# Optimization experiments

Hardware: AMD Instinct MI355X
Metric: run time of the kernel (lower is better)

Reference implementation:

```python
import jax, jax.numpy as jnp
import numpy as np

EPS_CR = 0.5      # eps in coding rate
ETA = 0.5
LAMBDA_LAP = 0.3
LN_EPS = 1e-5


def setup_inputs() -> dict:
    key = jax.random.key(0)
    ks = jax.random.split(key, 8)
    n, in_dim, out_dim, d_sub, K1 = 8192, 256, 128, 64, 3
    H = jax.random.normal(ks[0], (n, in_dim), jnp.float32)
    hop_feats = jax.random.normal(ks[1], (K1, n, in_dim), jnp.float32)
    L = jax.random.normal(ks[2], (n, n), jnp.float32) * 0.01
    W_stack = jax.random.normal(ks[3], (K1, d_sub, in_dim), jnp.float32) * 0.05
    W_out = jax.random.normal(ks[4], (out_dim, in_dim), jnp.float32) * 0.05
    threshold = jnp.full((out_dim,), 0.05, jnp.float32)
    ln_gamma = jnp.ones((out_dim,), jnp.float32)
    ln_beta = jnp.zeros((out_dim,), jnp.float32)
    tau = jnp.asarray(1.0, jnp.float32)
    return {"H": H, "hop_feats": hop_feats, "L": L, "W_stack": W_stack,
            "W_out": W_out, "threshold": threshold, "ln_gamma": ln_gamma,
            "ln_beta": ln_beta, "tau": tau}


def reference(H, hop_feats, L, W_stack, W_out, threshold, ln_gamma, ln_beta, tau):
    n = H.shape[0]
    d = W_stack.shape[1]
    coeff = d / (n * EPS_CR * EPS_CR)
    # per-hop subspace projections: Z [K+1, n, d]
    Z = jnp.einsum('knf,kdf->knd', hop_feats, W_stack)
    # shared Gram M = I + coeff * Z^T Z  [K+1, d, d]
    G = jnp.einsum('knd,kne->kde', Z, Z)
    M = jnp.eye(d, dtype=Z.dtype)[None] + coeff * G
    # coding rates via batched slogdet
    _, logdet = jnp.linalg.slogdet(M)
    R = 0.5 * logdet                                    # [K+1]
    # delta_R: first entry is R[0], rest are successive diffs
    delta_R = R - jnp.concatenate([jnp.zeros((1,), R.dtype), R[:-1]])
    dR_norm = (delta_R - delta_R.mean()) / (jnp.std(delta_R, ddof=1) + 1e-6)
    w = jax.nn.softmax(dR_norm / tau)                   # [K+1]
    # coding-rate gradients: g_Z = coeff * Z @ M^{-1} via batched solve
    g_Z = coeff * jnp.linalg.solve(M, jnp.swapaxes(Z, 1, 2))  # [K+1, d, n]
    # g_H[k] = g_Z[k]^T @ W[k]; weighted sum over hops -> [n, in_dim]
    grad_contrib = jnp.einsum('k,kdn,kdf->nf', w, g_Z, W_stack)
    H_half = H + ETA * grad_contrib - ETA * LAMBDA_LAP * (L @ H)
    # in_dim != out_dim -> project
    H_pre = H_half @ W_out.T                            # [n, out_dim]
    thr = jnp.abs(threshold)[None, :]
    H_soft = jnp.sign(H_pre) * jnp.maximum(jnp.abs(H_pre) - thr, 0.0)
    # LayerNorm over last dim
    mu = H_soft.mean(-1, keepdims=True)
    var = jnp.mean((H_soft - mu) ** 2, -1, keepdims=True)
    H_out = (H_soft - mu) * jax.lax.rsqrt(var + LN_EPS) * ln_gamma + ln_beta
    return (H_out, w, jax.lax.stop_gradient(dR_norm), jax.lax.stop_gradient(delta_R))
```

## Files before the change

kernel.cpp:

```cpp
#include <hip/hip_runtime.h>
#include <hip/hip_bf16.h>
#include <math.h>


#define COEFF 0.03125f
#define SCL_LAP (-0.15f)

typedef __attribute__((ext_vector_type(8))) short short8;
typedef __attribute__((ext_vector_type(4))) float f32x4;

__device__ __forceinline__ unsigned short f2bf_bits(float f) {
  unsigned int u = __float_as_uint(f);
  unsigned int r = (u + 0x7fffu + ((u >> 16) & 1u)) >> 16;
  return (unsigned short)r;
}

__global__ __launch_bounds__(256) void front_kernel(
    const float* __restrict__ H, const float* __restrict__ hop,
    const float* __restrict__ Wst, const float* __restrict__ Wout,
    float* __restrict__ Hp, unsigned short* __restrict__ HpT,
    float* __restrict__ Zbuf, float* __restrict__ Gpart,
    float* __restrict__ Pb) {
  __shared__ __align__(16) float smem[8704];
  float* As = smem;
  float* Bs = smem + 2112;
  const int tid = threadIdx.x;
  const int tx = tid & 15, ty = tid >> 4;
  const int b = blockIdx.x;

  const float* A;
  const float* B;
  int m0 = 0, k_id = 0, n_off = 0, mode;
  if (b < 192) {
    mode = 0; k_id = b >> 6; m0 = (b & 63) * 128;
    A = hop + (size_t)k_id * 2097152;
    B = Wst + (size_t)k_id * 16384;
  } else if (b < 320) {
    mode = 1; int i2 = b - 192;
    m0 = (i2 >> 1) * 128; n_off = (i2 & 1) * 64;
    A = H; B = Wout + (size_t)n_off * 256;
  } else {
    mode = 2; k_id = b - 320; m0 = 0;
    A = Wout; B = Wst + (size_t)k_id * 16384;
  }

  float acc[8][4];
#pragma unroll
  for (int i = 0; i < 8; ++i)
#pragma unroll
    for (int j = 0; j < 4; ++j) acc[i][j] = 0.f;

  const int arow = tid >> 1, ak = (tid & 1) * 8;
  const int brow = tid >> 2, bk = (tid & 3) * 4;
  for (int k0 = 0; k0 < 256; k0 += 16) {
    float4 a0 = *(const float4*)(A + (size_t)(m0 + arow) * 256 + k0 + ak);
    float4 a1 = *(const float4*)(A + (size_t)(m0 + arow) * 256 + k0 + ak + 4);
    float4 bv = *(const float4*)(B + (size_t)brow * 256 + k0 + bk);
    __syncthreads();
    As[(ak + 0) * 132 + arow] = a0.x; As[(ak + 1) * 132 + arow] = a0.y;
    As[(ak + 2) * 132 + arow] = a0.z; As[(ak + 3) * 132 + arow] = a0.w;
    As[(ak + 4) * 132 + arow] = a1.x; As[(ak + 5) * 132 + arow] = a1.y;
    As[(ak + 6) * 132 + arow] = a1.z; As[(ak + 7) * 132 + arow] = a1.w;
    Bs[(bk + 0) * 68 + brow] = bv.x; Bs[(bk + 1) * 68 + brow] = bv.y;
    Bs[(bk + 2) * 68 + brow] = bv.z; Bs[(bk + 3) * 68 + brow] = bv.w;
    __syncthreads();
#pragma unroll
    for (int kk = 0; kk < 16; ++kk) {
      float4 x0 = *(const float4*)&As[kk * 132 + ty * 8];
      float4 x1 = *(const float4*)&As[kk * 132 + ty * 8 + 4];
      float4 y4 = *(const float4*)&Bs[kk * 68 + tx * 4];
      float a8[8] = {x0.x, x0.y, x0.z, x0.w, x1.x, x1.y, x1.z, x1.w};
      float b4[4] = {y4.x, y4.y, y4.z, y4.w};
#pragma unroll
      for (int i = 0; i < 8; ++i)
#pragma unroll
        for (int j = 0; j < 4; ++j) acc[i][j] = fmaf(a8[i], b4[j], acc[i][j]);
    }
  }
  __syncthreads();

  if (mode == 0) {
#pragma unroll
    for (int i = 0; i < 8; ++i) {
      float4 v = {acc[i][0], acc[i][1], acc[i][2], acc[i][3]};
      *(float4*)(Zbuf + (size_t)(m0 + ty * 8 + i) * 192 + k_id * 64 + tx * 4) = v;
      *(float4*)&smem[(ty * 8 + i) * 68 + tx * 4] = v;
    }
    __syncthreads();
    float g[4][4];
#pragma unroll
    for (int i = 0; i < 4; ++i)
#pragma unroll
      for (int j = 0; j < 4; ++j) g[i][j] = 0.f;
    for (int r = 0; r < 128; ++r) {
      float4 zd4 = *(const float4*)&smem[r * 68 + ty * 4];
      float4 ze4 = *(const float4*)&smem[r * 68 + tx * 4];
      float zd[4] = {zd4.x, zd4.y, zd4.z, zd4.w};
      float ze[4] = {ze4.x, ze4.y, ze4.z, ze4.w};
#pragma unroll
      for (int i = 0; i < 4; ++i)
#pragma unroll
        for (int j = 0; j < 4; ++j) g[i][j] = fmaf(zd[i], ze[j], g[i][j]);
    }
    float* gp = Gpart + (size_t)(k_id * 64 + (b & 63)) * 4096;
#pragma unroll
    for (int i = 0; i < 4; ++i) {
      float4 v = {g[i][0], g[i][1], g[i][2], g[i][3]};
      *(float4*)(gp + (ty * 4 + i) * 64 + tx * 4) = v;
    }
  } else if (mode == 1) {
#pragma unroll
    for (int i = 0; i < 8; ++i) {
      float4 v = {acc[i][0], acc[i][1], acc[i][2], acc[i][3]};
      *(float4*)(Hp + (size_t)(m0 + ty * 8 + i) * 128 + n_off + tx * 4) = v;
      *(float4*)&smem[(ty * 8 + i) * 68 + tx * 4] = v;
    }
    __syncthreads();
    const int nn = tid >> 2, mc = (tid & 3) * 32;
    __attribute__((aligned(16))) unsigned short tmp[32];
#pragma unroll
    for (int mm = 0; mm < 32; ++mm) tmp[mm] = f2bf_bits(smem[(mc + mm) * 68 + nn]);
    unsigned short* dst = HpT + (size_t)(n_off + nn) * 8192 + m0 + mc;
    *(uint4*)(dst) = *(const uint4*)&tmp[0];
    *(uint4*)(dst + 8) = *(const uint4*)&tmp[8];
    *(uint4*)(dst + 16) = *(const uint4*)&tmp[16];
    *(uint4*)(dst + 24) = *(const uint4*)&tmp[24];
  } else {
    float* P = Pb + (size_t)k_id * 8192;
#pragma unroll
    for (int i = 0; i < 8; ++i) {
      float4 v = {acc[i][0], acc[i][1], acc[i][2], acc[i][3]};
      *(float4*)(P + (size_t)(ty * 8 + i) * 64 + tx * 4) = v;
    }
  }
}

__device__ __forceinline__ float blocksum256(float v, volatile float* scr) {
#pragma unroll
  for (int o = 32; o; o >>= 1) v += __shfl_xor(v, o);
  __syncthreads();
  if ((threadIdx.x & 63) == 0) scr[threadIdx.x >> 6] = v;
  __syncthreads();
  return scr[0] + scr[1] + scr[2] + scr[3];
}

__device__ __forceinline__ void gemm64s(const float* X, const float* Y,
                                        float acc[4][4]) {
  const int tx = threadIdx.x & 15, ty = threadIdx.x >> 4;
#pragma unroll
  for (int i = 0; i < 4; ++i)
#pragma unroll
    for (int j = 0; j < 4; ++j) acc[i][j] = 0.f;
  for (int kk = 0; kk < 64; ++kk) {
    float4 a4 = *(const float4*)&X[kk * 64 + ty * 4];
    float4 b4 = *(const float4*)&Y[kk * 64 + tx * 4];
    float a[4] = {a4.x, a4.y, a4.z, a4.w};
    float bb[4] = {b4.x, b4.y, b4.z, b4.w};
#pragma unroll
    for (int i = 0; i < 4; ++i)
#pragma unroll
      for (int j = 0; j < 4; ++j) acc[i][j] = fmaf(a[i], bb[j], acc[i][j]);
  }
}

__device__ __forceinline__ void wb64(float* D, const float acc[4][4]) {
  const int tx = threadIdx.x & 15, ty = threadIdx.x >> 4;
#pragma unroll
  for (int i = 0; i < 4; ++i)
#pragma unroll
    for (int j = 0; j < 4; ++j) D[(ty * 4 + i) * 64 + tx * 4 + j] = acc[i][j];
}

__device__ __forceinline__ float dot64(const float* X, const float* Y, float* scr) {
  const int tx = threadIdx.x & 15, ty = threadIdx.x >> 4;
  float v = 0.f;
#pragma unroll
  for (int i = 0; i < 4; ++i)
#pragma unroll
    for (int j = 0; j < 4; ++j) {
      int idx = (ty * 4 + i) * 64 + tx * 4 + j;
      v += X[idx] * Y[idx];
    }
  return blocksum256(v, scr);
}

__global__ __launch_bounds__(256) void fused_big(
    const float* __restrict__ Lp, const unsigned short* __restrict__ HpT,
    float* __restrict__ Pbuf, const float* __restrict__ Gpart,
    float* __restrict__ Minv, float* __restrict__ Rout) {
  __shared__ __align__(16) float smem[12304];
  const int tid = threadIdx.x;

  if (blockIdx.x >= 3) {
    unsigned short (*As)[40] = (unsigned short(*)[40])smem;
    unsigned short (*Bs)[40] = (unsigned short(*)[40])(smem + 2560);
    const int g = blockIdx.x - 3;
    const int split = g & 7;
    const int m0 = (g >> 3) * 128;
    const int kbase = split * 1024;
    const int wave = tid >> 6, lane = tid & 63;
    const int ar = tid >> 1, ah = (tid & 1) * 16;
    const size_t lrow = (size_t)(m0 + ar) * 8192;
    const size_t brow = (size_t)ar * 8192;
    f32x4 acc[2][8];
#pragma unroll
    for (int i = 0; i < 2; ++i)
#pragma unroll
      for (int j = 0; j < 8; ++j) acc[i][j] = (f32x4){0.f, 0.f, 0.f, 0.f};
    float4 apf[4];
    uint4 bpf[2];
    {
      const float* ap = Lp + lrow + kbase + ah;
      apf[0] = *(const float4*)(ap); apf[1] = *(const float4*)(ap + 4);
      apf[2] = *(const float4*)(ap + 8); apf[3] = *(const float4*)(ap + 12);
      const unsigned short* bp = HpT + brow + kbase + ah;
      bpf[0] = *(const uint4*)(bp); bpf[1] = *(const uint4*)(bp + 8);
    }
    const int quad = lane >> 4, mcol = lane & 15;
    for (int step = 0; step < 32; ++step) {
      __syncthreads();
      {
        __attribute__((aligned(16))) unsigned short tmp[16];
        const float* f = (const float*)apf;
#pragma unroll
        for (int i = 0; i < 16; ++i) tmp[i] = f2bf_bits(f[i]);
        *(uint4*)&As[ar][ah] = *(const uint4*)&tmp[0];
        *(uint4*)&As[ar][ah + 8] = *(const uint4*)&tmp[8];
        *(uint4*)&Bs[ar][ah] = bpf[0];
        *(uint4*)&Bs[ar][ah + 8] = bpf[1];
      }
      __syncthreads();
      if (step < 31) {
        int kc = kbase + (step + 1) * 32;
        const float* ap = Lp + lrow + kc + ah;
        apf[0] = *(const float4*)(ap); apf[1] = *(const float4*)(ap + 4);
        apf[2] = *(const float4*)(ap + 8); apf[3] = *(const float4*)(ap + 12);
        const unsigned short* bp = HpT + brow + kc + ah;
        bpf[0] = *(const uint4*)(bp); bpf[1] = *(const uint4*)(bp + 8);
      }
      short8 af0 = *(const short8*)&As[wave * 32 + mcol][quad * 8];
      short8 af1 = *(const short8*)&As[wave * 32 + 16 + mcol][quad * 8];
#pragma unroll
      for (int nt = 0; nt < 8; ++nt) {
        short8 bf = *(const short8*)&Bs[nt * 16 + mcol][quad * 8];
        acc[0][nt] = __builtin_amdgcn_mfma_f32_16x16x32_bf16(af0, bf, acc[0][nt], 0, 0, 0);
        acc[1][nt] = __builtin_amdgcn_mfma_f32_16x16x32_bf16(af1, bf, acc[1][nt], 0, 0, 0);
      }
    }
    float* P = Pbuf + (size_t)split * 1048576;
#pragma unroll
    for (int mt = 0; mt < 2; ++mt)
#pragma unroll
      for (int nt = 0; nt < 8; ++nt)
#pragma unroll
        for (int r = 0; r < 4; ++r) {
          int grow = m0 + wave * 32 + mt * 16 + quad * 4 + r;
          int gcol = nt * 16 + mcol;
          P[(size_t)grow * 128 + gcol] = acc[mt][nt][r];
        }
    return;
  }

  const int k = blockIdx.x;
  float* B0 = smem;
  float* B1 = smem + 4096;
  float* B2 = smem + 8192;
  float* scr = smem + 12288;
  for (int i4 = tid * 4; i4 < 4096; i4 += 1024) {
    const float* gp = Gpart + (size_t)k * 64 * 4096 + i4;
    float s0 = 0.f, s1 = 0.f, s2 = 0.f, s3 = 0.f;
    for (int bb2 = 0; bb2 < 64; ++bb2) {
      float4 v = *(const float4*)(gp + (size_t)bb2 * 4096);
      s0 += v.x; s1 += v.y; s2 += v.z; s3 += v.w;
    }
    float sv[4] = {s0, s1, s2, s3};
#pragma unroll
    for (int e = 0; e < 4; ++e) {
      int i = i4 + e;
      B0[i] = COEFF * sv[e] + ((i >> 6) == (i & 63) ? 1.f : 0.f);
    }
  }
  __syncthreads();
  if (tid < 64) {
    float rs = 0.f, dg = B0[tid * 65];
    for (int j = 0; j < 64; ++j) rs += fabsf(B0[j * 64 + tid]);
    float lo = 2.f * dg - rs, hi = rs;
#pragma unroll
    for (int o = 32; o; o >>= 1) {
      lo = fminf(lo, __shfl_xor(lo, o));
      hi = fmaxf(hi, __shfl_xor(hi, o));
    }
    if (tid == 0) scr[4] = 0.5f * (fmaxf(lo, 1.f) + hi);
  }
  __syncthreads();
  const float alpha = scr[4], inva = 1.f / alpha;
  for (int i = tid; i < 4096; i += 256) {
    int r = i >> 6, c = i & 63;
    B0[i] = B0[i] * inva - (r == c ? 1.f : 0.f);
  }
  __syncthreads();
  const int tx = tid & 15, ty = tid >> 4;
  float v1 = 0.f, v2 = 0.f;
#pragma unroll
  for (int i = 0; i < 4; ++i)
#pragma unroll
    for (int j = 0; j < 4; ++j) {
      int r = ty * 4 + i, c = tx * 4 + j;
      float e = B0[r * 64 + c];
      if (r == c) v1 += e;
      v2 += e * e;
    }
  float t1 = blocksum256(v1, scr);
  float t2 = blocksum256(v2, scr);
  float acc[4][4];
  gemm64s(B0, B0, acc); __syncthreads(); wb64(B1, acc); __syncthreads();
  float t3 = dot64(B1, B0, scr);
  float t4 = dot64(B1, B1, scr);
  gemm64s(B1, B0, acc); __syncthreads(); wb64(B2, acc); __syncthreads();
  float t5 = dot64(B2, B1, scr);
  float t6 = dot64(B2, B2, scr);
  gemm64s(B1, B1, acc);
  {
    float v7 = 0.f, v8 = 0.f;
#pragma unroll
    for (int i = 0; i < 4; ++i)
#pragma unroll
      for (int j = 0; j < 4; ++j) {
        int idx = (ty * 4 + i) * 64 + tx * 4 + j;
        v7 += acc[i][j] * B2[idx];
        v8 += acc[i][j] * acc[i][j];
      }
    float t7 = blocksum256(v7, scr);
    float t8 = blocksum256(v8, scr);
    if (tid == 0) {
      float ld = 64.f * logf(alpha) + t1 - t2 * 0.5f + t3 / 3.f - t4 * 0.25f
                 + t5 * 0.2f - t6 / 6.f + t7 / 7.f - t8 * 0.125f;
      Rout[k] = 0.5f * ld;
    }
  }
  for (int i = tid; i < 4096; i += 256) {
    int r = i >> 6, c = i & 63;
    B1[i] = (r == c ? 1.f : 0.f) - B0[i];
  }
  __syncthreads();
  for (int it = 0; it < 2; ++it) {
    gemm64s(B0, B1, acc);
    __syncthreads();
    {
#pragma unroll
      for (int i = 0; i < 4; ++i)
#pragma unroll
        for (int j = 0; j < 4; ++j) {
          int idx = (ty * 4 + i) * 64 + tx * 4 + j;
          B2[idx] = acc[i][j] + B1[idx];
        }
    }
    __syncthreads();
    gemm64s(B1, B2, acc);
    __syncthreads();
    {
#pragma unroll
      for (int i = 0; i < 4; ++i)
#pragma unroll
        for (int j = 0; j < 4; ++j) {
          int idx = (ty * 4 + i) * 64 + tx * 4 + j;
          B1[idx] = 2.f * B1[idx] - acc[i][j];
        }
    }
    __syncthreads();
  }
  for (int i = tid; i < 4096; i += 256) Minv[k * 4096 + i] = B1[i] * inva;
}

__global__ __launch_bounds__(256) void qtw_kernel(
    const float* __restrict__ Pb, const float* __restrict__ Minv,
    const float* __restrict__ R, const float* __restrict__ tauP,
    float* __restrict__ QT, float* __restrict__ tail) {
  __shared__ __align__(16) float XT[4096];
  __shared__ __align__(16) float Y[4096];
  __shared__ float wsh;
  const int tid = threadIdx.x;
  const int k = blockIdx.x >> 1;
  const int m0 = (blockIdx.x & 1) * 64;
  if (tid == 0) {
    float R0 = R[0], R1 = R[1], R2 = R[2];
    float d0 = R0, d1 = R1 - R0, d2 = R2 - R1;
    float mean = (d0 + d1 + d2) * (1.f / 3.f);
    float e0 = d0 - mean, e1 = d1 - mean, e2 = d2 - mean;
    float sd = sqrtf((e0 * e0 + e1 * e1 + e2 * e2) * 0.5f) + 1e-6f;
    float n0 = e0 / sd, n1 = e1 / sd, n2 = e2 / sd;
    float tau = tauP[0];
    float x0 = n0 / tau, x1 = n1 / tau, x2 = n2 / tau;
    float mx = fmaxf(x0, fmaxf(x1, x2));
    float w0 = expf(x0 - mx), w1 = expf(x1 - mx), w2 = expf(x2 - mx);
    float s = w0 + w1 + w2;
    w0 /= s; w1 /= s; w2 /= s;
    wsh = 0.015625f * (k == 0 ? w0 : (k == 1 ? w1 : w2));
    if (blockIdx.x == 0) {
      tail[0] = w0; tail[1] = w1; tail[2] = w2;
      tail[3] = n0; tail[4] = n1; tail[5] = n2;
      tail[6] = d0; tail[7] = d1; tail[8] = d2;
    }
  }
  {
    const int m = tid >> 2, c4 = (tid & 3) << 4;
    const float* src = Pb + (size_t)k * 8192 + (size_t)(m0 + m) * 64 + c4;
#pragma unroll
    for (int t = 0; t < 16; t += 4) {
      float4 v = *(const float4*)(src + t);
      XT[(c4 + t) * 64 + m] = v.x;
      XT[(c4 + t + 1) * 64 + m] = v.y;
      XT[(c4 + t + 2) * 64 + m] = v.z;
      XT[(c4 + t + 3) * 64 + m] = v.w;
    }
    for (int t = tid * 4; t < 4096; t += 1024)
      *(float4*)&Y[t] = *(const float4*)(Minv + (size_t)k * 4096 + t);
  }
  __syncthreads();
  float acc[4][4];
  gemm64s(XT, Y, acc);
  const float s = wsh;
  const int tx = tid & 15, ty = tid >> 4;
#pragma unroll
  for (int i = 0; i < 4; ++i) {
    float4 v = {s * acc[i][0], s * acc[i][1], s * acc[i][2], s * acc[i][3]};
    *(float4*)(QT + (size_t)(m0 + ty * 4 + i) * 192 + k * 64 + tx * 4) = v;
  }
}

__global__ __launch_bounds__(256) void back_kernel(
    const float* __restrict__ Zbuf, const float* __restrict__ QT,
    const float* __restrict__ Hp, const float* __restrict__ Pbuf,
    const float* __restrict__ thr, const float* __restrict__ gamma,
    const float* __restrict__ beta, float* __restrict__ out) {
  __shared__ __align__(16) float As[16][36];
  __shared__ __align__(16) float Bs[16][132];
  const int tid = threadIdx.x;
  const int tx = tid & 15, ty = tid >> 4;
  const int m0 = blockIdx.x * 32;
  float cc[2][8];
#pragma unroll
  for (int i = 0; i < 2; ++i)
#pragma unroll
    for (int j = 0; j < 8; ++j) cc[i][j] = 0.f;
  const int lr = tid >> 2, lc = (tid & 3) << 2;
  const int jr = tid >> 1, jc = (tid & 1) << 3;
  for (int k0 = 0; k0 < 192; k0 += 16) {
    if (tid < 128) {
      float4 av = *(const float4*)(Zbuf + (size_t)(m0 + lr) * 192 + k0 + lc);
      As[lc][lr] = av.x; As[lc + 1][lr] = av.y;
      As[lc + 2][lr] = av.z; As[lc + 3][lr] = av.w;
    }
    {
      const float* q = QT + (size_t)jr * 192 + k0 + jc;
      float4 b0 = *(const float4*)(q);
      float4 b1 = *(const float4*)(q + 4);
      Bs[jc][jr] = b0.x; Bs[jc + 1][jr] = b0.y;
      Bs[jc + 2][jr] = b0.z; Bs[jc + 3][jr] = b0.w;
      Bs[jc + 4][jr] = b1.x; Bs[jc + 5][jr] = b1.y;
      Bs[jc + 6][jr] = b1.z; Bs[jc + 7][jr] = b1.w;
    }
    __syncthreads();
#pragma unroll
    for (int kk = 0; kk < 16; ++kk) {
      float2 a2 = *(const float2*)&As[kk][ty * 2];
      float4 b4a = *(const float4*)&Bs[kk][tx * 8];
      float4 b4b = *(const float4*)&Bs[kk][tx * 8 + 4];
      float bb[8] = {b4a.x, b4a.y, b4a.z, b4a.w, b4b.x, b4b.y, b4b.z, b4b.w};
#pragma unroll
      for (int j = 0; j < 8; ++j) {
        cc[0][j] = fmaf(a2.x, bb[j], cc[0][j]);
        cc[1][j] = fmaf(a2.y, bb[j], cc[1][j]);
      }
    }
    __syncthreads();
  }
  const float4 tA = *(const float4*)(thr + tx * 8);
  const float4 tB = *(const float4*)(thr + tx * 8 + 4);
  const float tv[8] = {fabsf(tA.x), fabsf(tA.y), fabsf(tA.z), fabsf(tA.w),
                       fabsf(tB.x), fabsf(tB.y), fabsf(tB.z), fabsf(tB.w)};
  const float4 gA = *(const float4*)(gamma + tx * 8);
  const float4 gB = *(const float4*)(gamma + tx * 8 + 4);
  const float gv[8] = {gA.x, gA.y, gA.z, gA.w, gB.x, gB.y, gB.z, gB.w};
  const float4 bA = *(const float4*)(beta + tx * 8);
  const float4 bB = *(const float4*)(beta + tx * 8 + 4);
  const float bv[8] = {bA.x, bA.y, bA.z, bA.w, bB.x, bB.y, bB.z, bB.w};
  float sres[2][8], mean[2], inv[2];
#pragma unroll
  for (int i = 0; i < 2; ++i) {
    const size_t off = (size_t)(m0 + ty * 2 + i) * 128 + tx * 8;
    float4 h0 = *(const float4*)(Hp + off);
    float4 h1 = *(const float4*)(Hp + off + 4);
    float p[8] = {0.f, 0.f, 0.f, 0.f, 0.f, 0.f, 0.f, 0.f};
#pragma unroll
    for (int sp = 0; sp < 8; ++sp) {
      const float* pb = Pbuf + (size_t)sp * 1048576 + off;
      float4 q0 = *(const float4*)(pb);
      float4 q1 = *(const float4*)(pb + 4);
      p[0] += q0.x; p[1] += q0.y; p[2] += q0.z; p[3] += q0.w;
      p[4] += q1.x; p[5] += q1.y; p[6] += q1.z; p[7] += q1.w;
    }
    const float hv[8] = {h0.x, h0.y, h0.z, h0.w, h1.x, h1.y, h1.z, h1.w};
    float sum = 0.f;
#pragma unroll
    for (int j = 0; j < 8; ++j) {
      float x = cc[i][j] + hv[j] + SCL_LAP * p[j];
      float a = fmaxf(fabsf(x) - tv[j], 0.f);
      float sx = (x >= 0.f) ? a : -a;
      sres[i][j] = sx;
      sum += sx;
    }
#pragma unroll
    for (int o = 1; o < 16; o <<= 1) sum += __shfl_xor(sum, o);
    mean[i] = sum * (1.f / 128.f);
    float ss = 0.f;
#pragma unroll
    for (int j = 0; j < 8; ++j) {
      float dd = sres[i][j] - mean[i];
      ss += dd * dd;
    }
#pragma unroll
    for (int o = 1; o < 16; o <<= 1) ss += __shfl_xor(ss, o);
    inv[i] = rsqrtf(ss * (1.f / 128.f) + 1e-5f);
  }
#pragma unroll
  for (int i = 0; i < 2; ++i) {
    const size_t off = (size_t)(m0 + ty * 2 + i) * 128 + tx * 8;
    float o8[8];
#pragma unroll
    for (int j = 0; j < 8; ++j)
      o8[j] = (sres[i][j] - mean[i]) * inv[i] * gv[j] + bv[j];
    float4 v0 = {o8[0], o8[1], o8[2], o8[3]};
    float4 v1 = {o8[4], o8[5], o8[6], o8[7]};
    *(float4*)(out + off) = v0;
    *(float4*)(out + off + 4) = v1;
  }
}

extern "C" void kernel_launch(void* const* d_in, const int* in_sizes, int n_in,
                              void* d_out, int out_size, void* d_ws, size_t ws_size,
                              hipStream_t stream) {
  const float* H = (const float*)d_in[0];
  const float* hop = (const float*)d_in[1];
  const float* L = (const float*)d_in[2];
  const float* Wst = (const float*)d_in[3];
  const float* Wout = (const float*)d_in[4];
  const float* thr = (const float*)d_in[5];
  const float* gamma = (const float*)d_in[6];
  const float* beta = (const float*)d_in[7];
  const float* tau = (const float*)d_in[8];
  float* out = (float*)d_out;

  float* ws = (float*)d_ws;
  float* Zbuf = ws;
  float* Hp = Zbuf + 1572864;
  float* Gpart = Hp + 1048576;
  float* Minv = Gpart + 786432;
  float* Rb = Minv + 12288;
  float* Pb = Rb + 16;
  float* QT = Pb + 24576;
  float* Pbuf = QT + 24576;
  unsigned short* HpT = (unsigned short*)(Pbuf + 8388608);

  front_kernel<<<dim3(323), 256, 0, stream>>>(H, hop, Wst, Wout,
                                              Hp, HpT, Zbuf, Gpart, Pb);
  fused_big<<<dim3(515), 256, 0, stream>>>(L, HpT, Pbuf, Gpart, Minv, Rb);
  qtw_kernel<<<dim3(6), 256, 0, stream>>>(Pb, Minv, Rb, tau, QT, out + 1048576);
  back_kernel<<<dim3(256), 256, 0, stream>>>(Zbuf, QT, Hp, Pbuf,
                                             thr, gamma, beta, out);

  (void)in_sizes; (void)n_in; (void)out_size; (void)ws_size;
}
```

Measured before the change: 513.3 us.

## Pre-convert L to a tiled bf16 layout in the front kernel

The front kernel gains 512 extra blocks that read the fp32 Laplacian, round it to bf16 and write it into a tiled layout, one contiguous block per (row tile, k-split). This way each fused_big block streams a contiguous chunk. fused_big then loads those bf16 tiles straight into shared memory with no per-step conversion. Its block order also changes so consecutive blocks cover different row tiles of the same k-split, which may improve L2 reuse of HpT. The cost is an extra 128 MB write and read of the converted matrix, plus a larger workspace requirement that the code assumes is available.

Result: slower. 808.1 us (+57.4%).

```diff
diff --git a/kernel.cpp b/kernel.cpp
--- a/kernel.cpp
+++ b/kernel.cpp
@@ -18,29 +18,56 @@
 __global__ __launch_bounds__(256) void front_kernel(
     const float* __restrict__ H, const float* __restrict__ hop,
     const float* __restrict__ Wst, const float* __restrict__ Wout,
+    const float* __restrict__ L, unsigned short* __restrict__ Lt,
     float* __restrict__ Hp, unsigned short* __restrict__ HpT,
     float* __restrict__ Zbuf, float* __restrict__ Gpart,
     float* __restrict__ Pb) {
   __shared__ __align__(16) float smem[8704];
+  const int tid = threadIdx.x;
+  const int b = blockIdx.x;
+
+  if (b < 512) {
+    const int mt = b >> 3, ch = b & 7;
+    const float* Ls = L + (size_t)(mt * 128) * 8192 + ch * 1024;
+    unsigned short* Td = Lt + (size_t)b * 131072;
+    const int rr = tid >> 5, s = tid & 31;
+    const float* src0 = Ls + (size_t)rr * 8192 + s * 32;
+    unsigned short* dst0 = Td + (size_t)s * 4096 + rr * 32;
+    for (int it = 0; it < 16; ++it) {
+      const float* src = src0 + (size_t)(it * 8) * 8192;
+      float4 v[8];
+#pragma unroll
+      for (int q = 0; q < 8; ++q) v[q] = *(const float4*)(src + q * 4);
+      __attribute__((aligned(16))) unsigned short tmp[32];
+      const float* f = (const float*)v;
+#pragma unroll
+      for (int q = 0; q < 32; ++q) tmp[q] = f2bf_bits(f[q]);
+      unsigned short* dst = dst0 + it * 256;
+#pragma unroll
+      for (int q = 0; q < 4; ++q)
+        *(uint4*)(dst + q * 8) = *(const uint4*)&tmp[q * 8];
+    }
+    return;
+  }
+
   float* As = smem;
   float* Bs = smem + 2112;
-  const int tid = threadIdx.x;
   const int tx = tid & 15, ty = tid >> 4;
-  const int b = blockIdx.x;
 
   const float* A;
   const float* B;
-  int m0 = 0, k_id = 0, n_off = 0, mode;
-  if (b < 192) {
-    mode = 0; k_id = b >> 6; m0 = (b & 63) * 128;
+  int m0 = 0, k_id = 0, n_off = 0, mode, zidx = 0;
+  if (b < 704) {
+    mode = 0; zidx = b - 512;
+    k_id = zidx >> 6; m0 = (zidx & 63) * 128;
     A = hop + (size_t)k_id * 2097152;
     B = Wst + (size_t)k_id * 16384;
-  } else if (b < 320) {
-    mode = 1; int i2 = b - 192;
+  } else if (b < 832) {
+    mode = 1; int i2 = b - 704;
     m0 = (i2 >> 1) * 128; n_off = (i2 & 1) * 64;
     A = H; B = Wout + (size_t)n_off * 256;
   } else {
-    mode = 2; k_id = b - 320; m0 = 0;
+    mode = 2; k_id = b - 832; m0 = 0;
     A = Wout; B = Wst + (size_t)k_id * 16384;
   }
 
@@ -102,7 +129,7 @@
 #pragma unroll
         for (int j = 0; j < 4; ++j) g[i][j] = fmaf(zd[i], ze[j], g[i][j]);
     }
-    float* gp = Gpart + (size_t)(k_id * 64 + (b & 63)) * 4096;
+    float* gp = Gpart + (size_t)(k_id * 64 + (zidx & 63)) * 4096;
 #pragma unroll
     for (int i = 0; i < 4; ++i) {
       float4 v = {g[i][0], g[i][1], g[i][2], g[i][3]};
@@ -185,7 +212,7 @@
 }
 
 __global__ __launch_bounds__(256) void fused_big(
-    const float* __restrict__ Lp, const unsigned short* __restrict__ HpT,
+    const unsigned short* __restrict__ Lt, const unsigned short* __restrict__ HpT,
     float* __restrict__ Pbuf, const float* __restrict__ Gpart,
     float* __restrict__ Minv, float* __restrict__ Rout) {
   __shared__ __align__(16) float smem[12304];
@@ -195,24 +222,23 @@
     unsigned short (*As)[40] = (unsigned short(*)[40])smem;
     unsigned short (*Bs)[40] = (unsigned short(*)[40])(smem + 2560);
     const int g = blockIdx.x - 3;
-    const int split = g & 7;
-    const int m0 = (g >> 3) * 128;
-    const int kbase = split * 1024;
+    const int m_tile = g & 63;
+    const int split = g >> 6;
+    const int m0 = m_tile * 128;
     const int wave = tid >> 6, lane = tid & 63;
     const int ar = tid >> 1, ah = (tid & 1) * 16;
-    const size_t lrow = (size_t)(m0 + ar) * 8192;
+    const unsigned short* At = Lt + (size_t)(m_tile * 8 + split) * 131072 + tid * 16;
     const size_t brow = (size_t)ar * 8192;
+    const int kbase = split * 1024;
     f32x4 acc[2][8];
 #pragma unroll
     for (int i = 0; i < 2; ++i)
 #pragma unroll
       for (int j = 0; j < 8; ++j) acc[i][j] = (f32x4){0.f, 0.f, 0.f, 0.f};
-    float4 apf[4];
+    uint4 apf[2];
     uint4 bpf[2];
     {
-      const float* ap = Lp + lrow + kbase + ah;
-      apf[0] = *(const float4*)(ap); apf[1] = *(const float4*)(ap + 4);
-      apf[2] = *(const float4*)(ap + 8); apf[3] = *(const float4*)(ap + 12);
+      apf[0] = *(const uint4*)(At); apf[1] = *(const uint4*)(At + 8);
       const unsigned short* bp = HpT + brow + kbase + ah;
       bpf[0] = *(const uint4*)(bp); bpf[1] = *(const uint4*)(bp + 8);
     }
@@ -220,22 +246,16 @@
     for (int step = 0; step < 32; ++step) {
       __syncthreads();
       {
-        __attribute__((aligned(16))) unsigned short tmp[16];
-        const float* f = (const float*)apf;
-#pragma unroll
-        for (int i = 0; i < 16; ++i) tmp[i] = f2bf_bits(f[i]);
-        *(uint4*)&As[ar][ah] = *(const uint4*)&tmp[0];
-        *(uint4*)&As[ar][ah + 8] = *(const uint4*)&tmp[8];
+        *(uint4*)&As[ar][ah] = apf[0];
+        *(uint4*)&As[ar][ah + 8] = apf[1];
         *(uint4*)&Bs[ar][ah] = bpf[0];
         *(uint4*)&Bs[ar][ah + 8] = bpf[1];
       }
       __syncthreads();
       if (step < 31) {
-        int kc = kbase + (step + 1) * 32;
-        const float* ap = Lp + lrow + kc + ah;
-        apf[0] = *(const float4*)(ap); apf[1] = *(const float4*)(ap + 4);
-        apf[2] = *(const float4*)(ap + 8); apf[3] = *(const float4*)(ap + 12);
-        const unsigned short* bp = HpT + brow + kc + ah;
+        const unsigned short* ap = At + (size_t)(step + 1) * 4096;
+        apf[0] = *(const uint4*)(ap); apf[1] = *(const uint4*)(ap + 8);
+        const unsigned short* bp = HpT + brow + kbase + (step + 1) * 32 + ah;
         bpf[0] = *(const uint4*)(bp); bpf[1] = *(const uint4*)(bp + 8);
       }
       short8 af0 = *(const short8*)&As[wave * 32 + mcol][quad * 8];
@@ -561,10 +581,11 @@
   float* QT = Pb + 24576;
   float* Pbuf = QT + 24576;
   unsigned short* HpT = (unsigned short*)(Pbuf + 8388608);
-
-  front_kernel<<<dim3(323), 256, 0, stream>>>(H, hop, Wst, Wout,
+  unsigned short* Lt = HpT + 1048576;
+
+  front_kernel<<<dim3(835), 256, 0, stream>>>(H, hop, Wst, Wout, L, Lt,
                                               Hp, HpT, Zbuf, Gpart, Pb);
-  fused_big<<<dim3(515), 256, 0, stream>>>(L, HpT, Pbuf, Gpart, Minv, Rb);
+  fused_big<<<dim3(515), 256, 0, stream>>>(Lt, HpT, Pbuf, Gpart, Minv, Rb);
   qtw_kernel<<<dim3(6), 256, 0, stream>>>(Pb, Minv, Rb, tau, QT, out + 1048576);
   back_kernel<<<dim3(256), 256, 0, stream>>>(Zbuf, QT, Hp, Pbuf,
                                              thr, gamma, beta, out);
```
